# Performance work log

Hardware: AMD Instinct MI355X
Metric: run time of the kernel (lower is better)

## Reference

```python
import jax, jax.numpy as jnp
import numpy as np

GENOMES, BATCH, SEQ, EMBED = 8, 2, 2048, 1024
HEADS, KV_HEADS = 16, 4
HEAD_DIM = EMBED // HEADS  # 64
RATIO = HEADS // KV_HEADS  # 4
CONSTANT = 10000.0


def _rope_tables(seq_len, head_dim, constant):
    theta = constant ** (-2.0 * jnp.arange(0, head_dim, 2, dtype=jnp.float32) / head_dim)
    angles = jnp.arange(seq_len, dtype=jnp.float32)[:, None] * theta[None, :]  # [S, hd/2]
    return jnp.cos(angles), jnp.sin(angles)


def _apply_rope(x, cos, sin):
    # x: [g,b,s,h,hd]; treat last dim as hd/2 complex pairs, rotate by angle per (s, pair)
    g, b, s, h, hd = x.shape
    xr = x.reshape(g, b, s, h, hd // 2, 2)
    x0, x1 = xr[..., 0], xr[..., 1]
    c = cos[None, None, :, None, :]
    sn = sin[None, None, :, None, :]
    o0 = x0 * c - x1 * sn
    o1 = x0 * sn + x1 * c
    return jnp.stack([o0, o1], axis=-1).reshape(g, b, s, h, hd)


def setup_inputs() -> dict:
    key = jax.random.key(0)
    ks = jax.random.split(key, 5)
    scale = 0.02
    return {
        "tensor": jax.random.normal(ks[0], (GENOMES, BATCH, SEQ, EMBED), dtype=jnp.float32),
        "Wq": jax.random.normal(ks[1], (GENOMES, EMBED, HEADS * HEAD_DIM), dtype=jnp.float32) * scale,
        "Wk": jax.random.normal(ks[2], (GENOMES, EMBED, KV_HEADS * HEAD_DIM), dtype=jnp.float32) * scale,
        "Wv": jax.random.normal(ks[3], (GENOMES, EMBED, KV_HEADS * HEAD_DIM), dtype=jnp.float32) * scale,
        "Wo": jax.random.normal(ks[4], (GENOMES, EMBED, EMBED), dtype=jnp.float32) * scale,
    }


def reference(tensor, Wq, Wk, Wv, Wo):
    g, b, s, _ = tensor.shape
    cos, sin = _rope_tables(SEQ, HEAD_DIM, CONSTANT)
    # per-genome linear projections
    q = jnp.einsum('gbsi,gio->gbso', tensor, Wq).reshape(g, b, s, HEADS, HEAD_DIM)
    k = jnp.einsum('gbsi,gio->gbso', tensor, Wk).reshape(g, b, s, KV_HEADS, HEAD_DIM)
    v = jnp.einsum('gbsi,gio->gbso', tensor, Wv).reshape(g, b, s, KV_HEADS, HEAD_DIM)
    q = _apply_rope(q, cos, sin)
    k = _apply_rope(k, cos, sin)
    # repeat_kv: [g,b,s,kvh,hd] -> [g,b,s,kvh*ratio,hd]
    k = jnp.broadcast_to(k[:, :, :, :, None, :], (g, b, s, KV_HEADS, RATIO, HEAD_DIM)).reshape(g, b, s, HEADS, HEAD_DIM)
    v = jnp.broadcast_to(v[:, :, :, :, None, :], (g, b, s, KV_HEADS, RATIO, HEAD_DIM)).reshape(g, b, s, HEADS, HEAD_DIM)
    # NOTE: faithful to the original (non-standard) einsums: contraction over seq in QK^T,
    # energy is [g,b,h,head_dim,head_dim]
    energy = jnp.einsum('gbshq,gbshk->gbhqk', q, k)
    scores = jax.nn.softmax(energy / jnp.sqrt(jnp.float32(HEAD_DIM)), axis=-1)
    # attention = value scaled by total score mass per (g,b,h)
    attention = jnp.einsum('gbhqk,gbshv->gbshv', scores, v)
    attention = attention.reshape(g, b, s, EMBED)
    return jnp.einsum('gbsi,gio->gbso', attention, Wo)
```

## Files before the change

### kernel.cpp

```cpp
#include <hip/hip_runtime.h>
#include <stdint.h>

#define GENOMES 8
#define BATCH 2
#define SEQ 2048
#define EMBED 1024
#define KVD 256
#define M_PER_G (BATCH*SEQ)

typedef float f32x4 __attribute__((ext_vector_type(4)));
typedef __bf16 bf16x8 __attribute__((ext_vector_type(8)));
typedef short s16x8 __attribute__((ext_vector_type(8)));
typedef short s16x4 __attribute__((ext_vector_type(4)));

static __device__ __forceinline__ unsigned short f2bf(float f) {
  unsigned int u = __builtin_bit_cast(unsigned int, f);
  u += 0x7FFFu + ((u >> 16) & 1u);
  return (unsigned short)(u >> 16);
}

static __device__ __forceinline__ void gll16(const void* g, void* l) {
  __builtin_amdgcn_global_load_lds(
      (const __attribute__((address_space(1))) unsigned int*)g,
      (__attribute__((address_space(3))) unsigned int*)l, 16, 0, 0);
}

#define WAITVM(n) asm volatile("s_waitcnt vmcnt(" #n ")" ::: "memory")
#define MEMFENCE() asm volatile("" ::: "memory")

__global__ __launch_bounds__(256) void wvt_kernel(const float* __restrict__ Wv,
                                                  unsigned short* __restrict__ WvT) {
  int g = blockIdx.y;
  int it = blockIdx.x >> 2;
  int ot = blockIdx.x & 3;
  int i0 = it * 64, o0 = ot * 64;
  const float* W = Wv + (size_t)g * EMBED * KVD;
  unsigned short* T = WvT + (size_t)g * KVD * EMBED;
  __shared__ unsigned short tl[64][65];
  int t = threadIdx.x;
  int rr = t >> 4;
  int cc = (t & 15) * 4;
#pragma unroll
  for (int p = 0; p < 4; ++p) {
    int r = rr + p * 16;
    float4 v = *(const float4*)(W + (size_t)(i0 + r) * KVD + o0 + cc);
    tl[r][cc + 0] = f2bf(v.x);
    tl[r][cc + 1] = f2bf(v.y);
    tl[r][cc + 2] = f2bf(v.z);
    tl[r][cc + 3] = f2bf(v.w);
  }
  __syncthreads();
#pragma unroll
  for (int p = 0; p < 4; ++p) {
    int o = rr + p * 16;
    s16x4 v;
    v[0] = (short)tl[cc + 0][o];
    v[1] = (short)tl[cc + 1][o];
    v[2] = (short)tl[cc + 2][o];
    v[3] = (short)tl[cc + 3][o];
    *(s16x4*)(T + (size_t)(o0 + o) * EMBED + i0 + cc) = v;
  }
}

__global__ __launch_bounds__(256) void rt_kernel(const float* __restrict__ Wo,
                                                 unsigned short* __restrict__ RT) {
  int g = blockIdx.y;
  int ot = blockIdx.x >> 2;
  int kh = blockIdx.x & 3;
  int o0 = ot * 64;
  const float* W = Wo + (size_t)g * EMBED * EMBED;
  unsigned short* T = RT + (size_t)g * EMBED * KVD;
  __shared__ float tl[64][65];
  int t = threadIdx.x;
  int rr = t >> 4;
  int cc = (t & 15) * 4;
#pragma unroll
  for (int p = 0; p < 4; ++p) {
    int d = rr + p * 16;
    float a0 = 0.f, a1 = 0.f, a2 = 0.f, a3 = 0.f;
#pragma unroll
    for (int r = 0; r < 4; ++r) {
      float4 v = *(const float4*)(W + (size_t)(kh * 256 + r * 64 + d) * EMBED + o0 + cc);
      a0 += v.x; a1 += v.y; a2 += v.z; a3 += v.w;
    }
    tl[d][cc + 0] = a0; tl[d][cc + 1] = a1; tl[d][cc + 2] = a2; tl[d][cc + 3] = a3;
  }
  __syncthreads();
#pragma unroll
  for (int p = 0; p < 4; ++p) {
    int o = rr + p * 16;
    s16x4 v;
    v[0] = (short)f2bf(64.f * tl[cc + 0][o]);
    v[1] = (short)f2bf(64.f * tl[cc + 1][o]);
    v[2] = (short)f2bf(64.f * tl[cc + 2][o]);
    v[3] = (short)f2bf(64.f * tl[cc + 3][o]);
    *(s16x4*)(T + (size_t)(o0 + o) * KVD + kh * 64 + cc) = v;
  }
}

template <bool A_F32, bool OUT_BF16, int M, int N, int K>
__global__ __launch_bounds__(256) void gemm_bt(const void* __restrict__ Aall,
                                               const unsigned short* __restrict__ Btall,
                                               void* __restrict__ Call) {
  constexpr int BM = 128, BN = 64, BK = 32;
  constexpr int ABYTES = A_F32 ? BM * BK * 4 : BM * BK * 2;
  constexpr int SB = ABYTES + BN * BK * 2;
  constexpr int NTN = N / BN;
  constexpr int NWG = (M / BM) * NTN;
  constexpr int NT = K / BK;
  static_assert(NWG % 8 == 0, "XCD swizzle needs nwg%8==0");
  static_assert(NT >= 4, "pipeline depth 4 needs NT>=4");

  __shared__ __align__(16) unsigned char smem[4 * SB];

  int g = blockIdx.y;
  int bid = blockIdx.x;
  int lt = (bid & 7) * (NWG >> 3) + (bid >> 3);
  int bm = lt / NTN, bn = lt % NTN;
  int m0 = bm * BM, n0 = bn * BN;

  const unsigned short* Bt = Btall + (size_t)g * N * K;
  const float* Af = (const float*)Aall + (size_t)g * M * K;
  const unsigned short* Ab = (const unsigned short*)Aall + (size_t)g * M * K;

  int tid = threadIdx.x;
  int lane = tid & 63, wave = tid >> 6;
  int lm = lane & 15, quad = lane >> 4;
  int wm = wave * 32;

  const float* srcAf = nullptr;
  const unsigned short* srcAb = nullptr;
  if constexpr (A_F32) {
    int rA = wave * 8 + (lane >> 3);
    int cA = (lane & 7) ^ (rA & 7);
    srcAf = Af + (size_t)(m0 + rA) * K + cA * 4;
  } else {
    int rA = wave * 16 + (lane >> 2);
    int cA = (lane & 3) ^ ((rA >> 1) & 3);
    srcAb = Ab + (size_t)(m0 + rA) * K + cA * 8;
  }
  int rB = wave * 16 + (lane >> 2);
  int cB = (lane & 3) ^ ((rB >> 1) & 3);
  const unsigned short* srcB = Bt + (size_t)(n0 + rB) * K + cB * 8;

  int offA[2][2];
  int offB[4];
#pragma unroll
  for (int i = 0; i < 2; ++i) {
    if constexpr (A_F32) {
#pragma unroll
      for (int u = 0; u < 2; ++u)
        offA[i][u] = (wm + i * 16 + lm) * 128 + (((2 * quad + u) ^ (lm & 7)) * 16);
    } else {
      offA[i][0] = (wm + i * 16 + lm) * 64 + ((quad ^ ((lm >> 1) & 3)) * 16);
    }
  }
#pragma unroll
  for (int j = 0; j < 4; ++j)
    offB[j] = ABYTES + (j * 16 + lm) * 64 + ((quad ^ ((lm >> 1) & 3)) * 16);

  f32x4 acc[2][4] = {};

  auto stage = [&](int slot, int t) {
    unsigned char* db = smem + slot * SB;
    if constexpr (A_F32) {
      const float* s = srcAf + t * BK;
#pragma unroll
      for (int p = 0; p < 4; ++p)
        gll16(s + (size_t)p * 32 * K, db + p * 4096 + wave * 1024);
    } else {
      const unsigned short* s = srcAb + t * BK;
#pragma unroll
      for (int p = 0; p < 2; ++p)
        gll16(s + (size_t)p * 64 * K, db + p * 4096 + wave * 1024);
    }
    gll16(srcB + t * BK, db + ABYTES + wave * 1024);
  };

  auto iter_body = [&](int t) {
    const unsigned char* db = smem + (t & 3) * SB;
    bf16x8 a[2], b[4];
    if constexpr (A_F32) {
#pragma unroll
      for (int i = 0; i < 2; ++i) {
        f32x4 lo = *(const f32x4*)(db + offA[i][0]);
        f32x4 hi = *(const f32x4*)(db + offA[i][1]);
#pragma unroll
        for (int u = 0; u < 4; ++u) {
          a[i][u] = (__bf16)lo[u];
          a[i][4 + u] = (__bf16)hi[u];
        }
      }
    } else {
#pragma unroll
      for (int i = 0; i < 2; ++i)
        a[i] = __builtin_bit_cast(bf16x8, *(const s16x8*)(db + offA[i][0]));
    }
#pragma unroll
    for (int j = 0; j < 4; ++j)
      b[j] = __builtin_bit_cast(bf16x8, *(const s16x8*)(db + offB[j]));

    if (t + 3 < NT) stage((t + 3) & 3, t + 3);

#pragma unroll
    for (int i = 0; i < 2; ++i)
#pragma unroll
      for (int j = 0; j < 4; ++j)
        acc[i][j] = __builtin_amdgcn_mfma_f32_16x16x32_bf16(a[i], b[j], acc[i][j], 0, 0, 0);
  };

  stage(0, 0);
  stage(1, 1);
  stage(2, 2);

  for (int t = 0; t < NT - 2; ++t) {
    if constexpr (A_F32) WAITVM(10); else WAITVM(6);
    __builtin_amdgcn_s_barrier();
    MEMFENCE();
    iter_body(t);
  }
  {
    if constexpr (A_F32) WAITVM(5); else WAITVM(3);
    __builtin_amdgcn_s_barrier();
    MEMFENCE();
    iter_body(NT - 2);
  }
  {
    WAITVM(0);
    __builtin_amdgcn_s_barrier();
    MEMFENCE();
    iter_body(NT - 1);
  }

  if constexpr (OUT_BF16) {
    unsigned short* C = (unsigned short*)Call + (size_t)g * M * N;
#pragma unroll
    for (int i = 0; i < 2; ++i)
#pragma unroll
      for (int j = 0; j < 4; ++j)
#pragma unroll
        for (int r = 0; r < 4; ++r) {
          int mm = m0 + wm + i * 16 + quad * 4 + r;
          int nn = n0 + j * 16 + lm;
          C[(size_t)mm * N + nn] = f2bf(acc[i][j][r]);
        }
  } else {
    float* C = (float*)Call + (size_t)g * M * N;
#pragma unroll
    for (int i = 0; i < 2; ++i)
#pragma unroll
      for (int j = 0; j < 4; ++j)
#pragma unroll
        for (int r = 0; r < 4; ++r) {
          int mm = m0 + wm + i * 16 + quad * 4 + r;
          int nn = n0 + j * 16 + lm;
          C[(size_t)mm * N + nn] = acc[i][j][r];
        }
  }
}

extern "C" void kernel_launch(void* const* d_in, const int* in_sizes, int n_in,
                              void* d_out, int out_size, void* d_ws, size_t ws_size,
                              hipStream_t stream) {
  const float* tensor = (const float*)d_in[0];
  const float* Wv = (const float*)d_in[3];
  const float* Wo = (const float*)d_in[4];
  float* out = (float*)d_out;

  unsigned short* WvT = (unsigned short*)d_ws;
  unsigned short* RT  = WvT + (size_t)GENOMES * KVD * EMBED;
  unsigned short* V   = RT  + (size_t)GENOMES * EMBED * KVD;

  wvt_kernel<<<dim3(64, GENOMES), 256, 0, stream>>>(Wv, WvT);
  rt_kernel<<<dim3(64, GENOMES), 256, 0, stream>>>(Wo, RT);

  gemm_bt<true, true, M_PER_G, KVD, EMBED>
      <<<dim3((M_PER_G / 128) * (KVD / 64), GENOMES), 256, 0, stream>>>(tensor, WvT, V);

  gemm_bt<false, false, M_PER_G, EMBED, KVD>
      <<<dim3((M_PER_G / 128) * (EMBED / 64), GENOMES), 256, 0, stream>>>(V, RT, out);
}
```

Measured before the change: 326.2 us.

## Fold Wv into output weight and enlarge GEMM tiles to 128x128

Reassociates the product so that Wv·R is formed first as a per-genome 1024x1024 bf16 weight, and the input is multiplied by it once. This removes the intermediate V buffer round-trip and the transposing Wv kernel, which is replaced by a flat cast. It roughly doubles the main GEMM's FLOPs. The GEMM tile also grows to 128x128 with a 2x2 wave layout and a 3-stage rather than 4-stage LDS pipeline, trading occupancy and LDS for more reuse per tile.

New measurement: 377.8 us. 1.16x slower.

```diff
diff --git a/kernel.cpp b/kernel.cpp
--- a/kernel.cpp
+++ b/kernel.cpp
@@ -28,38 +28,17 @@
 #define WAITVM(n) asm volatile("s_waitcnt vmcnt(" #n ")" ::: "memory")
 #define MEMFENCE() asm volatile("" ::: "memory")
 
-__global__ __launch_bounds__(256) void wvt_kernel(const float* __restrict__ Wv,
-                                                  unsigned short* __restrict__ WvT) {
-  int g = blockIdx.y;
-  int it = blockIdx.x >> 2;
-  int ot = blockIdx.x & 3;
-  int i0 = it * 64, o0 = ot * 64;
-  const float* W = Wv + (size_t)g * EMBED * KVD;
-  unsigned short* T = WvT + (size_t)g * KVD * EMBED;
-  __shared__ unsigned short tl[64][65];
-  int t = threadIdx.x;
-  int rr = t >> 4;
-  int cc = (t & 15) * 4;
-#pragma unroll
-  for (int p = 0; p < 4; ++p) {
-    int r = rr + p * 16;
-    float4 v = *(const float4*)(W + (size_t)(i0 + r) * KVD + o0 + cc);
-    tl[r][cc + 0] = f2bf(v.x);
-    tl[r][cc + 1] = f2bf(v.y);
-    tl[r][cc + 2] = f2bf(v.z);
-    tl[r][cc + 3] = f2bf(v.w);
-  }
-  __syncthreads();
-#pragma unroll
-  for (int p = 0; p < 4; ++p) {
-    int o = rr + p * 16;
-    s16x4 v;
-    v[0] = (short)tl[cc + 0][o];
-    v[1] = (short)tl[cc + 1][o];
-    v[2] = (short)tl[cc + 2][o];
-    v[3] = (short)tl[cc + 3][o];
-    *(s16x4*)(T + (size_t)(o0 + o) * EMBED + i0 + cc) = v;
-  }
+__global__ __launch_bounds__(256) void castwv_kernel(const float* __restrict__ Wv,
+                                                     unsigned short* __restrict__ O) {
+  size_t i = ((size_t)blockIdx.x * 256 + threadIdx.x) * 8;
+  f32x4 a = *(const f32x4*)(Wv + i);
+  f32x4 b = *(const f32x4*)(Wv + i + 4);
+  s16x8 o;
+  o[0] = (short)f2bf(a[0]); o[1] = (short)f2bf(a[1]);
+  o[2] = (short)f2bf(a[2]); o[3] = (short)f2bf(a[3]);
+  o[4] = (short)f2bf(b[0]); o[5] = (short)f2bf(b[1]);
+  o[6] = (short)f2bf(b[2]); o[7] = (short)f2bf(b[3]);
+  *(s16x8*)(O + i) = o;
 }
 
 __global__ __launch_bounds__(256) void rt_kernel(const float* __restrict__ Wo,
@@ -102,16 +81,16 @@
 __global__ __launch_bounds__(256) void gemm_bt(const void* __restrict__ Aall,
                                                const unsigned short* __restrict__ Btall,
                                                void* __restrict__ Call) {
-  constexpr int BM = 128, BN = 64, BK = 32;
+  constexpr int BM = 128, BN = 128, BK = 32;
   constexpr int ABYTES = A_F32 ? BM * BK * 4 : BM * BK * 2;
   constexpr int SB = ABYTES + BN * BK * 2;
   constexpr int NTN = N / BN;
   constexpr int NWG = (M / BM) * NTN;
   constexpr int NT = K / BK;
   static_assert(NWG % 8 == 0, "XCD swizzle needs nwg%8==0");
-  static_assert(NT >= 4, "pipeline depth 4 needs NT>=4");
-
-  __shared__ __align__(16) unsigned char smem[4 * SB];
+  static_assert(NT >= 3, "pipeline needs NT>=3");
+
+  __shared__ __align__(16) unsigned char smem[3 * SB];
 
   int g = blockIdx.y;
   int bid = blockIdx.x;
@@ -126,7 +105,7 @@
   int tid = threadIdx.x;
   int lane = tid & 63, wave = tid >> 6;
   int lm = lane & 15, quad = lane >> 4;
-  int wm = wave * 32;
+  int wm = (wave >> 1) * 64, wn = (wave & 1) * 64;
 
   const float* srcAf = nullptr;
   const unsigned short* srcAb = nullptr;
@@ -135,18 +114,18 @@
     int cA = (lane & 7) ^ (rA & 7);
     srcAf = Af + (size_t)(m0 + rA) * K + cA * 4;
   } else {
-    int rA = wave * 16 + (lane >> 2);
+    int rA = wave * 32 + (lane >> 2);
     int cA = (lane & 3) ^ ((rA >> 1) & 3);
     srcAb = Ab + (size_t)(m0 + rA) * K + cA * 8;
   }
-  int rB = wave * 16 + (lane >> 2);
+  int rB = wave * 32 + (lane >> 2);
   int cB = (lane & 3) ^ ((rB >> 1) & 3);
   const unsigned short* srcB = Bt + (size_t)(n0 + rB) * K + cB * 8;
 
-  int offA[2][2];
+  int offA[4][2];
   int offB[4];
 #pragma unroll
-  for (int i = 0; i < 2; ++i) {
+  for (int i = 0; i < 4; ++i) {
     if constexpr (A_F32) {
 #pragma unroll
       for (int u = 0; u < 2; ++u)
@@ -157,32 +136,35 @@
   }
 #pragma unroll
   for (int j = 0; j < 4; ++j)
-    offB[j] = ABYTES + (j * 16 + lm) * 64 + ((quad ^ ((lm >> 1) & 3)) * 16);
-
-  f32x4 acc[2][4] = {};
+    offB[j] = ABYTES + (wn + j * 16 + lm) * 64 + ((quad ^ ((lm >> 1) & 3)) * 16);
+
+  f32x4 acc[4][4] = {};
 
   auto stage = [&](int slot, int t) {
     unsigned char* db = smem + slot * SB;
     if constexpr (A_F32) {
-      const float* s = srcAf + t * BK;
+      const float* s = srcAf + (size_t)t * BK;
 #pragma unroll
       for (int p = 0; p < 4; ++p)
-        gll16(s + (size_t)p * 32 * K, db + p * 4096 + wave * 1024);
+        gll16(s + (size_t)p * 32 * K, db + wave * 1024 + p * 4096);
     } else {
-      const unsigned short* s = srcAb + t * BK;
+      const unsigned short* s = srcAb + (size_t)t * BK;
 #pragma unroll
       for (int p = 0; p < 2; ++p)
-        gll16(s + (size_t)p * 64 * K, db + p * 4096 + wave * 1024);
-    }
-    gll16(srcB + t * BK, db + ABYTES + wave * 1024);
+        gll16(s + (size_t)p * 16 * K, db + wave * 2048 + p * 1024);
+    }
+    const unsigned short* s = srcB + (size_t)t * BK;
+#pragma unroll
+    for (int p = 0; p < 2; ++p)
+      gll16(s + (size_t)p * 16 * K, db + ABYTES + wave * 2048 + p * 1024);
   };
 
-  auto iter_body = [&](int t) {
-    const unsigned char* db = smem + (t & 3) * SB;
-    bf16x8 a[2], b[4];
+  auto iter_body = [&](int rd, int wr, int t) {
+    const unsigned char* db = smem + rd * SB;
+    bf16x8 a[4], b[4];
     if constexpr (A_F32) {
 #pragma unroll
-      for (int i = 0; i < 2; ++i) {
+      for (int i = 0; i < 4; ++i) {
         f32x4 lo = *(const f32x4*)(db + offA[i][0]);
         f32x4 hi = *(const f32x4*)(db + offA[i][1]);
 #pragma unroll
@@ -193,17 +175,17 @@
       }
     } else {
 #pragma unroll
-      for (int i = 0; i < 2; ++i)
+      for (int i = 0; i < 4; ++i)
         a[i] = __builtin_bit_cast(bf16x8, *(const s16x8*)(db + offA[i][0]));
     }
 #pragma unroll
     for (int j = 0; j < 4; ++j)
       b[j] = __builtin_bit_cast(bf16x8, *(const s16x8*)(db + offB[j]));
 
-    if (t + 3 < NT) stage((t + 3) & 3, t + 3);
-
-#pragma unroll
-    for (int i = 0; i < 2; ++i)
+    if (t + 2 < NT) stage(wr, t + 2);
+
+#pragma unroll
+    for (int i = 0; i < 4; ++i)
 #pragma unroll
       for (int j = 0; j < 4; ++j)
         acc[i][j] = __builtin_amdgcn_mfma_f32_16x16x32_bf16(a[i], b[j], acc[i][j], 0, 0, 0);
@@ -211,49 +193,45 @@
 
   stage(0, 0);
   stage(1, 1);
-  stage(2, 2);
-
-  for (int t = 0; t < NT - 2; ++t) {
-    if constexpr (A_F32) WAITVM(10); else WAITVM(6);
+
+  int rd = 0, wr = 2;
+  for (int t = 0; t < NT - 1; ++t) {
+    if constexpr (A_F32) WAITVM(6); else WAITVM(4);
     __builtin_amdgcn_s_barrier();
     MEMFENCE();
-    iter_body(t);
-  }
-  {
-    if constexpr (A_F32) WAITVM(5); else WAITVM(3);
-    __builtin_amdgcn_s_barrier();
-    MEMFENCE();
-    iter_body(NT - 2);
+    iter_body(rd, wr, t);
+    rd = (rd == 2) ? 0 : rd + 1;
+    wr = (wr == 2) ? 0 : wr + 1;
   }
   {
     WAITVM(0);
     __builtin_amdgcn_s_barrier();
     MEMFENCE();
-    iter_body(NT - 1);
+    iter_body(rd, wr, NT - 1);
   }
 
   if constexpr (OUT_BF16) {
     unsigned short* C = (unsigned short*)Call + (size_t)g * M * N;
 #pragma unroll
-    for (int i = 0; i < 2; ++i)
+    for (int i = 0; i < 4; ++i)
 #pragma unroll
       for (int j = 0; j < 4; ++j)
 #pragma unroll
         for (int r = 0; r < 4; ++r) {
           int mm = m0 + wm + i * 16 + quad * 4 + r;
-          int nn = n0 + j * 16 + lm;
+          int nn = n0 + wn + j * 16 + lm;
           C[(size_t)mm * N + nn] = f2bf(acc[i][j][r]);
         }
   } else {
     float* C = (float*)Call + (size_t)g * M * N;
 #pragma unroll
-    for (int i = 0; i < 2; ++i)
+    for (int i = 0; i < 4; ++i)
 #pragma unroll
       for (int j = 0; j < 4; ++j)
 #pragma unroll
         for (int r = 0; r < 4; ++r) {
           int mm = m0 + wm + i * 16 + quad * 4 + r;
-          int nn = n0 + j * 16 + lm;
+          int nn = n0 + wn + j * 16 + lm;
           C[(size_t)mm * N + nn] = acc[i][j][r];
         }
   }
@@ -267,16 +245,16 @@
   const float* Wo = (const float*)d_in[4];
   float* out = (float*)d_out;
 
-  unsigned short* WvT = (unsigned short*)d_ws;
-  unsigned short* RT  = WvT + (size_t)GENOMES * KVD * EMBED;
-  unsigned short* V   = RT  + (size_t)GENOMES * EMBED * KVD;
-
-  wvt_kernel<<<dim3(64, GENOMES), 256, 0, stream>>>(Wv, WvT);
+  unsigned short* WvB  = (unsigned short*)d_ws;
+  unsigned short* RT   = WvB  + (size_t)GENOMES * EMBED * KVD;
+  unsigned short* Wful = RT   + (size_t)GENOMES * EMBED * KVD;
+
+  castwv_kernel<<<dim3(GENOMES * EMBED * KVD / (256 * 8)), 256, 0, stream>>>(Wv, WvB);
   rt_kernel<<<dim3(64, GENOMES), 256, 0, stream>>>(Wo, RT);
 
-  gemm_bt<true, true, M_PER_G, KVD, EMBED>
-      <<<dim3((M_PER_G / 128) * (KVD / 64), GENOMES), 256, 0, stream>>>(tensor, WvT, V);
-
-  gemm_bt<false, false, M_PER_G, EMBED, KVD>
-      <<<dim3((M_PER_G / 128) * (EMBED / 64), GENOMES), 256, 0, stream>>>(V, RT, out);
-}
+  gemm_bt<false, true, EMBED, EMBED, KVD>
+      <<<dim3((EMBED / 128) * (EMBED / 128), GENOMES), 256, 0, stream>>>(RT, WvB, Wful);
+
+  gemm_bt<true, false, M_PER_G, EMBED, EMBED>
+      <<<dim3((M_PER_G / 128) * (EMBED / 128), GENOMES), 256, 0, stream>>>(tensor, Wful, out);
+}
```
